# Performance work log

Measured on AMD Instinct MI355X. Metric: run time of the kernel, lower is better.

## Reference

```python
import jax, jax.numpy as jnp
import numpy as np

B, S, H = 64, 512, 256
H2 = 2 * H
TOPK, TRUNC = 5, 100
EPS = 1e-7
TMAX = S + 1  # h_old slot 0 is the initial zero state; one slot appended per step
NEG = -1e9


def setup_inputs() -> dict:
    key = jax.random.key(0)
    ks = jax.random.split(key, 8)
    p = lambda k, shape: jax.random.normal(k, shape, jnp.float32) * 0.08
    return {
        "x": jax.random.normal(ks[0], (B, S), jnp.float32),
        "W_ih_f": p(ks[1], (4 * H, 1)),
        "W_hh_f": p(ks[2], (4 * H, H)),
        "b_f": p(ks[3], (4 * H,)),
        "W_ih_b": p(ks[4], (4 * H, 1)),
        "W_hh_b": p(ks[5], (4 * H, H)),
        "b_b": p(ks[6], (4 * H,)),
        "w_t": p(ks[7], (4 * H, 1)),
    }


def _lstm_cell(xt, h, c, W_ih, W_hh, b):
    # torch.nn.LSTMCell: gates ordered i, f, g, o
    g = xt @ W_ih.T + h @ W_hh.T + b
    i, f, gg, o = jnp.split(g, 4, axis=1)
    i, f, o = jax.nn.sigmoid(i), jax.nn.sigmoid(f), jax.nn.sigmoid(o)
    c2 = f * c + i * jnp.tanh(gg)
    return o * jnp.tanh(c2), c2


def _forward(x, W_ih_f, W_hh_f, b_f, W_ih_b, W_hh_b, b_b, w_t):
    # tanh(cat(h_comb, h_old)) @ w_t == tanh(h_comb)@w1 + tanh(h_old)@w2
    w1, w2 = w_t[:H2, 0], w_t[H2:, 0]
    pos = jnp.arange(TMAX)

    h0 = jnp.zeros((B, H), jnp.float32)
    h_old0 = jnp.zeros((B, TMAX, H2), jnp.float32)   # slot 0 = initial zeros (valid)
    th_old0 = jnp.zeros((B, TMAX, H2), jnp.float32)  # cached tanh(h_old)
    carry0 = (h0, h0, h0, h0, h_old0, th_old0,
              jnp.zeros((B, H2), jnp.float32), jnp.zeros((B, TMAX), jnp.float32))

    def step(carry, i):
        h_f, c_f, h_b, c_b, h_old, th_old, _, _ = carry
        trunc = ((i + 1) % TRUNC) == 0  # TBPTT detach point
        sg = lambda a: jnp.where(trunc, jax.lax.stop_gradient(a), a)
        h_f, c_f, h_b, c_b = sg(h_f), sg(c_f), sg(h_b), sg(c_b)

        xf = jax.lax.dynamic_slice_in_dim(x, i, 1, axis=1)          # [B,1]
        xb = jax.lax.dynamic_slice_in_dim(x, S - 1 - i, 1, axis=1)  # [B,1]
        h_f, c_f = _lstm_cell(xf, h_f, c_f, W_ih_f, W_hh_f, b_f)
        h_b, c_b = _lstm_cell(xb, h_b, c_b, W_ih_b, W_hh_b, b_b)
        h_comb = jnp.concatenate([h_f, h_b], axis=1)  # [B,2H]

        rs = i + 1                    # remember_size before append
        valid = pos < rs              # [TMAX]
        s = jnp.tanh(h_comb) @ w1[:, None] + th_old @ w2  # [B,1]+[B,TMAX]
        s_m = jnp.where(valid[None, :], s, NEG)

        # Sparse_attention: subtract k-th largest, clamp at 0, renormalize
        delta = jax.lax.top_k(s_m, TOPK)[0][:, -1] + EPS  # [B]
        w_sp = jnp.clip(s_m - delta[:, None], 0.0, None)
        w_sp = w_sp / (w_sp.sum(axis=1, keepdims=True) + EPS)
        w_raw = jnp.where(valid[None, :], s, 0.0)  # time_step <= top_k branch
        attn_w = jnp.where(rs <= TOPK, w_raw, w_sp)  # [B,TMAX]

        attn_c = jnp.einsum('bt,bth->bh', attn_w, h_old)  # weighted sum of cache
        h_new = h_comb + attn_c

        h_old = jax.lax.dynamic_update_slice_in_dim(
            h_old, h_new[:, None, :], i + 1, axis=1)
        th_old = jax.lax.dynamic_update_slice_in_dim(
            th_old, jnp.tanh(h_new)[:, None, :], i + 1, axis=1)
        return (h_f, c_f, h_b, c_b, h_old, th_old, attn_c, attn_w), None

    carry, _ = jax.lax.scan(step, carry0, jnp.arange(S))
    attn_c, attn_w = carry[6], carry[7]
    # last step: remember_size == S, torch returns [B, S, 1]
    return attn_c, attn_w[:, :S, None]


def reference(x, W_ih_f, W_hh_f, b_f, W_ih_b, W_hh_b, b_b, w_t):
    return _forward(x, W_ih_f, W_hh_f, b_f, W_ih_b, W_hh_b, b_b, w_t)
```

## Files before the change

### kernel.cpp

```cpp
#include <hip/hip_runtime.h>
#include <math.h>

#define BB    64
#define SS    512
#define HH    256
#define HH2   512
#define TMAXX 513
#define NTOP  5
#define EPSF  1e-7f

#if defined(__has_builtin)
#if __has_builtin(__builtin_amdgcn_sdot4)
#define HAVE_SDOT4 1
#endif
#endif

__device__ __forceinline__ int dot4i8_(unsigned a, int b, int c) {
#ifdef HAVE_SDOT4
  return __builtin_amdgcn_sdot4((int)a, b, c, false);
#else
  int acc = c;
#pragma unroll
  for (int j = 0; j < 4; ++j) {
    int av = (int)(signed char)(a >> (8 * j));
    int bv = (int)(signed char)(((unsigned)b) >> (8 * j));
    acc += av * bv;
  }
  return acc;
#endif
}


__global__ void init_kernel(const float* __restrict__ Whh_f, const float* __restrict__ Whh_b,
                            uint4* __restrict__ wq, float* __restrict__ scales) {
  int t = blockIdx.x * blockDim.x + threadIdx.x;
  if (t >= 2048) return;
  int d = t >> 10, row = t & 1023;
  const float* src = (d ? Whh_b : Whh_f) + (size_t)row * HH;
  float m = 1e-20f;
  for (int k = 0; k < HH; ++k) m = fmaxf(m, fabsf(src[k]));
  float inv = 127.f / m;
  scales[t] = m * (1.f / 16129.f);
  for (int kq4 = 0; kq4 < 16; ++kq4) {
    unsigned u[4];
#pragma unroll
    for (int w = 0; w < 4; ++w) {
      unsigned uu = 0;
#pragma unroll
      for (int j = 0; j < 4; ++j) {
        float q = rintf(src[kq4 * 16 + w * 4 + j] * inv);
        q = fminf(fmaxf(q, -127.f), 127.f);
        uu |= ((unsigned)(((int)q) & 0xff)) << (8 * j);
      }
      u[w] = uu;
    }
    wq[(size_t)(d * 16 + kq4) * 1024 + row] = make_uint4(u[0], u[1], u[2], u[3]);
  }
}

__global__ __launch_bounds__(1024, 4)
void lstm_kernel(const float* __restrict__ x,
                 const float* __restrict__ wihf, const float* __restrict__ bf,
                 const float* __restrict__ wihb, const float* __restrict__ bb_,
                 const uint4* __restrict__ wq, const float* __restrict__ scales,
                 float* __restrict__ hcomb) {
  const int r   = blockIdx.x >> 1;
  const int d   = blockIdx.x & 1;
  const int tid = threadIdx.x;

  __shared__ float x_lds[SS];
  __shared__ float gates_lds[1024];
  __shared__ int   h_ints[64];

  for (int t = tid; t < SS; t += 1024) x_lds[t] = x[(size_t)r * SS + t];
  if (tid < 64) h_ints[tid] = 0;

  const float wihv = d ? wihb[tid] : wihf[tid];
  const float bv   = d ? bb_[tid]  : bf[tid];
  const float sc   = scales[d * 1024 + tid];
  float c = 0.f;
  float* hout = hcomb + (size_t)r * SS * HH2 + d * HH;

  uint4 w[16];
  {
    const uint4* wbase = wq + (size_t)(d * 16) * 1024 + tid;
#pragma unroll
    for (int q = 0; q < 16; ++q) w[q] = wbase[(size_t)q * 1024];
  }
  __syncthreads();

  for (int i = 0; i < SS; ++i) {
    int a0 = 0, a1 = 0, a2 = 0, a3 = 0;
    const int4* hp = (const int4*)h_ints;
#pragma unroll
    for (int q = 0; q < 16; ++q) {
      int4 h4 = hp[q];
      a0 = dot4i8_(w[q].x, h4.x, a0);
      a1 = dot4i8_(w[q].y, h4.y, a1);
      a2 = dot4i8_(w[q].z, h4.z, a2);
      a3 = dot4i8_(w[q].w, h4.w, a3);
    }
    float xv = x_lds[d ? (SS - 1 - i) : i];
    gates_lds[tid] = (float)(a0 + a1 + a2 + a3) * sc + fmaf(xv, wihv, bv);
    __syncthreads();
    if (tid < HH) {
      float gi = gates_lds[tid];
      float gf = gates_lds[HH + tid];
      float gg = gates_lds[2 * HH + tid];
      float go = gates_lds[3 * HH + tid];
      float ig = 1.f / (1.f + expf(-gi));
      float fg = 1.f / (1.f + expf(-gf));
      float og = 1.f / (1.f + expf(-go));
      c = fg * c + ig * tanhf(gg);
      float hn = og * tanhf(c);
      hout[(size_t)i * HH2 + tid] = hn;
      ((signed char*)h_ints)[tid] = (signed char)(int)rintf(hn * 127.f);
    }
    __syncthreads();
  }
}

__global__ __launch_bounds__(512, 1)
void attn_kernel(const float* __restrict__ w_t, float* __restrict__ hcomb,
                 float* __restrict__ out) {
  const int b = blockIdx.x;
  const int e = threadIdx.x;
  const int lane = e & 63, wv = e >> 6;
  float* hrow = hcomb + (size_t)b * SS * HH2;

  __shared__ float w1_l[HH2], w2_l[HH2];
  __shared__ float tw_l[TMAXX];
  __shared__ float t5v[NTOP];
  __shared__ int   t5i[NTOP];
  __shared__ float redp[8];
  __shared__ float sh_s1, sh_tw5, sh_inv;
  __shared__ float sh_wk[4];
  __shared__ int   sh_ik[4];

  w1_l[e] = w_t[e];
  w2_l[e] = w_t[HH2 + e];
  if (e == 0) { tw_l[0] = 0.f; t5v[0] = 0.f; t5i[0] = 0; }
  int t5cnt = 1;
  __syncthreads();

  for (int i = 0; i < SS; ++i) {
    float hc = hrow[(size_t)i * HH2 + e];
    if (i < NTOP) {
      float v = tanhf(hc) * w1_l[e];
#pragma unroll
      for (int m = 32; m >= 1; m >>= 1) v += __shfl_xor(v, m, 64);
      if (lane == 0) redp[wv] = v;
      __syncthreads();
      if (e == 0) {
        float s = 0.f;
#pragma unroll
        for (int q = 0; q < 8; ++q) s += redp[q];
        sh_s1 = s;
      }
    }
    if (i >= NTOP && e == 0) {
      float tw5 = t5v[4];
      float rk[4], rsum = 0.f;
#pragma unroll
      for (int k = 0; k < 4; ++k) {
        float rr = t5v[k] - tw5 - EPSF;
        rk[k] = rr > 0.f ? rr : 0.f;
        rsum += rk[k];
      }
      float inv = 1.f / (rsum + EPSF);
#pragma unroll
      for (int k = 0; k < 4; ++k) { sh_wk[k] = rk[k] * inv; sh_ik[k] = t5i[k]; }
      sh_tw5 = tw5; sh_inv = inv;
    }
    __syncthreads();
    float acc = 0.f;
    if (i >= NTOP) {
#pragma unroll
      for (int k = 0; k < 4; ++k) {
        float w = sh_wk[k];
        int   t = sh_ik[k];
        if (w > 0.f && t > 0)
          acc = fmaf(w, hrow[(size_t)(t - 1) * HH2 + e], acc);
      }
    } else {
      float s1 = sh_s1;
      for (int t = 1; t <= i; ++t)
        acc = fmaf(s1 + tw_l[t], hrow[(size_t)(t - 1) * HH2 + e], acc);
    }
    float hn = hc + acc;
    hrow[(size_t)i * HH2 + e] = hn;
    float v2 = tanhf(hn) * w2_l[e];
#pragma unroll
    for (int m = 32; m >= 1; m >>= 1) v2 += __shfl_xor(v2, m, 64);
    if (lane == 0) redp[wv] = v2;
    if (i == SS - 1) {
      out[(size_t)b * HH2 + e] = acc;
      float rr = tw_l[e] - sh_tw5 - EPSF;
      out[(size_t)BB * HH2 + (size_t)b * SS + e] = rr > 0.f ? rr * sh_inv : 0.f;
    }
    __syncthreads();
    if (e == 0) {
      float v = 0.f;
#pragma unroll
      for (int q = 0; q < 8; ++q) v += redp[q];
      int idx = i + 1;
      tw_l[idx] = v;
      if (t5cnt < NTOP) {
        int p = t5cnt++;
        t5v[p] = v; t5i[p] = idx;
        while (p > 0 && t5v[p] > t5v[p - 1]) {
          float tv = t5v[p]; t5v[p] = t5v[p - 1]; t5v[p - 1] = tv;
          int   ti = t5i[p]; t5i[p] = t5i[p - 1]; t5i[p - 1] = ti;
          --p;
        }
      } else if (v > t5v[4]) {
        t5v[4] = v; t5i[4] = idx;
        int p = 4;
        while (p > 0 && t5v[p] > t5v[p - 1]) {
          float tv = t5v[p]; t5v[p] = t5v[p - 1]; t5v[p - 1] = tv;
          int   ti = t5i[p]; t5i[p] = t5i[p - 1]; t5i[p - 1] = ti;
          --p;
        }
      }
    }
    __syncthreads();
  }
}

extern "C" void kernel_launch(void* const* d_in, const int* in_sizes, int n_in,
                              void* d_out, int out_size, void* d_ws, size_t ws_size,
                              hipStream_t stream) {
  const float* x     = (const float*)d_in[0];
  const float* Wih_f = (const float*)d_in[1];
  const float* Whh_f = (const float*)d_in[2];
  const float* b_f   = (const float*)d_in[3];
  const float* Wih_b = (const float*)d_in[4];
  const float* Whh_b = (const float*)d_in[5];
  const float* b_b   = (const float*)d_in[6];
  const float* w_t   = (const float*)d_in[7];
  float* out = (float*)d_out;

  char* ws = (char*)d_ws;
  uint4*  wq     = (uint4*)ws;
  float*  scales = (float*)(ws + (1 << 20));
  float*  hcomb  = (float*)(ws + (4 << 20));

  init_kernel<<<8, 256, 0, stream>>>(Whh_f, Whh_b, wq, scales);
  lstm_kernel<<<2 * BB, 1024, 0, stream>>>(x, Wih_f, b_f, Wih_b, b_b,
                                           wq, scales, hcomb);
  attn_kernel<<<BB, 512, 0, stream>>>(w_t, hcomb, out);
}
```

Before: 1.346 ms.

## Restructure LSTM to one thread per hidden unit and attention to single-wave registers

After: 1.445 ms. +7.3%, slower.

```diff
diff --git a/kernel.cpp b/kernel.cpp
--- a/kernel.cpp
+++ b/kernel.cpp
@@ -58,172 +58,187 @@
   }
 }
 
-__global__ __launch_bounds__(1024, 4)
+__global__ __launch_bounds__(256, 1)
 void lstm_kernel(const float* __restrict__ x,
                  const float* __restrict__ wihf, const float* __restrict__ bf,
                  const float* __restrict__ wihb, const float* __restrict__ bb_,
                  const uint4* __restrict__ wq, const float* __restrict__ scales,
                  float* __restrict__ hcomb) {
-  const int r   = blockIdx.x >> 1;
-  const int d   = blockIdx.x & 1;
-  const int tid = threadIdx.x;
+  const int r = blockIdx.x >> 1;
+  const int d = blockIdx.x & 1;
+  const int e = threadIdx.x;
 
   __shared__ float x_lds[SS];
-  __shared__ float gates_lds[1024];
-  __shared__ int   h_ints[64];
-
-  for (int t = tid; t < SS; t += 1024) x_lds[t] = x[(size_t)r * SS + t];
-  if (tid < 64) h_ints[tid] = 0;
-
-  const float wihv = d ? wihb[tid] : wihf[tid];
-  const float bv   = d ? bb_[tid]  : bf[tid];
-  const float sc   = scales[d * 1024 + tid];
+  __shared__ int   hbuf[2][64];
+
+  for (int t = e; t < SS; t += 256) x_lds[t] = x[(size_t)r * SS + t];
+  if (e < 64) hbuf[0][e] = 0;
+
+  float wih[4], bias[4], sc[4];
+#pragma unroll
+  for (int g = 0; g < 4; ++g) {
+    int row = g * HH + e;
+    wih[g]  = d ? wihb[row] : wihf[row];
+    bias[g] = d ? bb_[row]  : bf[row];
+    sc[g]   = scales[d * 1024 + row];
+  }
+  uint4 w[4][16];
+#pragma unroll
+  for (int g = 0; g < 4; ++g) {
+    const uint4* wb = wq + (size_t)(d * 16) * 1024 + g * HH + e;
+#pragma unroll
+    for (int q = 0; q < 16; ++q) w[g][q] = wb[(size_t)q * 1024];
+  }
   float c = 0.f;
   float* hout = hcomb + (size_t)r * SS * HH2 + d * HH;
-
-  uint4 w[16];
-  {
-    const uint4* wbase = wq + (size_t)(d * 16) * 1024 + tid;
-#pragma unroll
-    for (int q = 0; q < 16; ++q) w[q] = wbase[(size_t)q * 1024];
-  }
   __syncthreads();
 
+  int cur = 0;
   for (int i = 0; i < SS; ++i) {
+    const int4* hp = (const int4*)hbuf[cur];
     int a0 = 0, a1 = 0, a2 = 0, a3 = 0;
-    const int4* hp = (const int4*)h_ints;
 #pragma unroll
     for (int q = 0; q < 16; ++q) {
       int4 h4 = hp[q];
-      a0 = dot4i8_(w[q].x, h4.x, a0);
-      a1 = dot4i8_(w[q].y, h4.y, a1);
-      a2 = dot4i8_(w[q].z, h4.z, a2);
-      a3 = dot4i8_(w[q].w, h4.w, a3);
+      a0 = dot4i8_(w[0][q].x, h4.x, a0); a0 = dot4i8_(w[0][q].y, h4.y, a0);
+      a0 = dot4i8_(w[0][q].z, h4.z, a0); a0 = dot4i8_(w[0][q].w, h4.w, a0);
+      a1 = dot4i8_(w[1][q].x, h4.x, a1); a1 = dot4i8_(w[1][q].y, h4.y, a1);
+      a1 = dot4i8_(w[1][q].z, h4.z, a1); a1 = dot4i8_(w[1][q].w, h4.w, a1);
+      a2 = dot4i8_(w[2][q].x, h4.x, a2); a2 = dot4i8_(w[2][q].y, h4.y, a2);
+      a2 = dot4i8_(w[2][q].z, h4.z, a2); a2 = dot4i8_(w[2][q].w, h4.w, a2);
+      a3 = dot4i8_(w[3][q].x, h4.x, a3); a3 = dot4i8_(w[3][q].y, h4.y, a3);
+      a3 = dot4i8_(w[3][q].z, h4.z, a3); a3 = dot4i8_(w[3][q].w, h4.w, a3);
     }
     float xv = x_lds[d ? (SS - 1 - i) : i];
-    gates_lds[tid] = (float)(a0 + a1 + a2 + a3) * sc + fmaf(xv, wihv, bv);
+    float gi = (float)a0 * sc[0] + fmaf(xv, wih[0], bias[0]);
+    float gf = (float)a1 * sc[1] + fmaf(xv, wih[1], bias[1]);
+    float gg = (float)a2 * sc[2] + fmaf(xv, wih[2], bias[2]);
+    float go = (float)a3 * sc[3] + fmaf(xv, wih[3], bias[3]);
+    float ig = 1.f / (1.f + expf(-gi));
+    float fg = 1.f / (1.f + expf(-gf));
+    float og = 1.f / (1.f + expf(-go));
+    c = fg * c + ig * tanhf(gg);
+    float hn = og * tanhf(c);
+    hout[(size_t)i * HH2 + e] = hn;
+    ((signed char*)hbuf[cur ^ 1])[e] = (signed char)(int)rintf(hn * 127.f);
+    cur ^= 1;
     __syncthreads();
-    if (tid < HH) {
-      float gi = gates_lds[tid];
-      float gf = gates_lds[HH + tid];
-      float gg = gates_lds[2 * HH + tid];
-      float go = gates_lds[3 * HH + tid];
-      float ig = 1.f / (1.f + expf(-gi));
-      float fg = 1.f / (1.f + expf(-gf));
-      float og = 1.f / (1.f + expf(-go));
-      c = fg * c + ig * tanhf(gg);
-      float hn = og * tanhf(c);
-      hout[(size_t)i * HH2 + tid] = hn;
-      ((signed char*)h_ints)[tid] = (signed char)(int)rintf(hn * 127.f);
-    }
-    __syncthreads();
-  }
-}
-
-__global__ __launch_bounds__(512, 1)
-void attn_kernel(const float* __restrict__ w_t, float* __restrict__ hcomb,
+  }
+}
+
+__global__ __launch_bounds__(64, 1)
+void attn_kernel(const float* __restrict__ w_t, const float* __restrict__ hcomb,
                  float* __restrict__ out) {
   const int b = blockIdx.x;
-  const int e = threadIdx.x;
-  const int lane = e & 63, wv = e >> 6;
-  float* hrow = hcomb + (size_t)b * SS * HH2;
-
-  __shared__ float w1_l[HH2], w2_l[HH2];
+  const int l = threadIdx.x;
+  const float* hrow = hcomb + (size_t)b * SS * HH2;
+
   __shared__ float tw_l[TMAXX];
-  __shared__ float t5v[NTOP];
-  __shared__ int   t5i[NTOP];
-  __shared__ float redp[8];
-  __shared__ float sh_s1, sh_tw5, sh_inv;
-  __shared__ float sh_wk[4];
-  __shared__ int   sh_ik[4];
-
-  w1_l[e] = w_t[e];
-  w2_l[e] = w_t[HH2 + e];
-  if (e == 0) { tw_l[0] = 0.f; t5v[0] = 0.f; t5i[0] = 0; }
-  int t5cnt = 1;
-  __syncthreads();
+
+  const float4 w1a = *(const float4*)(w_t + 4 * l);
+  const float4 w1b = *(const float4*)(w_t + HH + 4 * l);
+  const float4 w2a = *(const float4*)(w_t + HH2 + 4 * l);
+  const float4 w2b = *(const float4*)(w_t + HH2 + HH + 4 * l);
+
+  float t5v[5] = {0.f, -1e30f, -1e30f, -1e30f, -1e30f};
+  int   t5s[5] = {0, 1, 2, 3, 4};
+  int   t5cnt  = 1;
+  float4 z4 = make_float4(0.f, 0.f, 0.f, 0.f);
+  float4 sA0 = z4, sA1 = z4, sA2 = z4, sA3 = z4, sA4 = z4;
+  float4 sB0 = z4, sB1 = z4, sB2 = z4, sB3 = z4, sB4 = z4;
+  if (l == 0) tw_l[0] = 0.f;
+
+  float4 ha = *(const float4*)(hrow + 4 * l);
+  float4 hb = *(const float4*)(hrow + HH + 4 * l);
+  float tw5 = 0.f, inv = 0.f;
+  float4 aA = z4, aB = z4;
 
   for (int i = 0; i < SS; ++i) {
-    float hc = hrow[(size_t)i * HH2 + e];
-    if (i < NTOP) {
-      float v = tanhf(hc) * w1_l[e];
-#pragma unroll
-      for (int m = 32; m >= 1; m >>= 1) v += __shfl_xor(v, m, 64);
-      if (lane == 0) redp[wv] = v;
-      __syncthreads();
-      if (e == 0) {
-        float s = 0.f;
-#pragma unroll
-        for (int q = 0; q < 8; ++q) s += redp[q];
-        sh_s1 = s;
+    float4 na = z4, nb = z4;
+    if (i + 1 < SS) {
+      na = *(const float4*)(hrow + (size_t)(i + 1) * HH2 + 4 * l);
+      nb = *(const float4*)(hrow + (size_t)(i + 1) * HH2 + HH + 4 * l);
+    }
+    float wr[5];
+    if (i >= NTOP) {
+      tw5 = t5v[4];
+      float rk0 = fmaxf(t5v[0] - tw5 - EPSF, 0.f);
+      float rk1 = fmaxf(t5v[1] - tw5 - EPSF, 0.f);
+      float rk2 = fmaxf(t5v[2] - tw5 - EPSF, 0.f);
+      float rk3 = fmaxf(t5v[3] - tw5 - EPSF, 0.f);
+      inv = 1.f / (rk0 + rk1 + rk2 + rk3 + EPSF);
+      wr[0] = rk0 * inv; wr[1] = rk1 * inv; wr[2] = rk2 * inv; wr[3] = rk3 * inv;
+      wr[4] = 0.f;
+    } else {
+      float s = tanhf(ha.x) * w1a.x + tanhf(ha.y) * w1a.y +
+                tanhf(ha.z) * w1a.z + tanhf(ha.w) * w1a.w +
+                tanhf(hb.x) * w1b.x + tanhf(hb.y) * w1b.y +
+                tanhf(hb.z) * w1b.z + tanhf(hb.w) * w1b.w;
+#pragma unroll
+      for (int m = 1; m < 64; m <<= 1) s += __shfl_xor(s, m, 64);
+#pragma unroll
+      for (int k = 0; k < 5; ++k) wr[k] = (k < t5cnt) ? (s + t5v[k]) : 0.f;
+    }
+    float ws0 = 0.f, ws1 = 0.f, ws2 = 0.f, ws3 = 0.f, ws4 = 0.f;
+#pragma unroll
+    for (int k = 0; k < 5; ++k) {
+      float wv = wr[k]; int s2 = t5s[k];
+      ws0 += (s2 == 0) ? wv : 0.f;
+      ws1 += (s2 == 1) ? wv : 0.f;
+      ws2 += (s2 == 2) ? wv : 0.f;
+      ws3 += (s2 == 3) ? wv : 0.f;
+      ws4 += (s2 == 4) ? wv : 0.f;
+    }
+    aA.x = ws0*sA0.x + ws1*sA1.x + ws2*sA2.x + ws3*sA3.x + ws4*sA4.x;
+    aA.y = ws0*sA0.y + ws1*sA1.y + ws2*sA2.y + ws3*sA3.y + ws4*sA4.y;
+    aA.z = ws0*sA0.z + ws1*sA1.z + ws2*sA2.z + ws3*sA3.z + ws4*sA4.z;
+    aA.w = ws0*sA0.w + ws1*sA1.w + ws2*sA2.w + ws3*sA3.w + ws4*sA4.w;
+    aB.x = ws0*sB0.x + ws1*sB1.x + ws2*sB2.x + ws3*sB3.x + ws4*sB4.x;
+    aB.y = ws0*sB0.y + ws1*sB1.y + ws2*sB2.y + ws3*sB3.y + ws4*sB4.y;
+    aB.z = ws0*sB0.z + ws1*sB1.z + ws2*sB2.z + ws3*sB3.z + ws4*sB4.z;
+    aB.w = ws0*sB0.w + ws1*sB1.w + ws2*sB2.w + ws3*sB3.w + ws4*sB4.w;
+    float4 hnA, hnB;
+    hnA.x = ha.x + aA.x; hnA.y = ha.y + aA.y; hnA.z = ha.z + aA.z; hnA.w = ha.w + aA.w;
+    hnB.x = hb.x + aB.x; hnB.y = hb.y + aB.y; hnB.z = hb.z + aB.z; hnB.w = hb.w + aB.w;
+    float v = tanhf(hnA.x) * w2a.x + tanhf(hnA.y) * w2a.y +
+              tanhf(hnA.z) * w2a.z + tanhf(hnA.w) * w2a.w +
+              tanhf(hnB.x) * w2b.x + tanhf(hnB.y) * w2b.y +
+              tanhf(hnB.z) * w2b.z + tanhf(hnB.w) * w2b.w;
+#pragma unroll
+    for (int m = 1; m < 64; m <<= 1) v += __shfl_xor(v, m, 64);
+    if (l == 0) tw_l[i + 1] = v;
+    bool full = (t5cnt >= 5);
+    bool ins  = !full || (v > t5v[4]);
+    if (ins) {
+      int p    = full ? 4 : t5cnt;
+      int slot = full ? t5s[4] : t5cnt;
+#pragma unroll
+      for (int k = 0; k < 5; ++k) if (k == p) { t5v[k] = v; t5s[k] = slot; }
+      if (slot == 0)      { sA0 = hnA; sB0 = hnB; }
+      else if (slot == 1) { sA1 = hnA; sB1 = hnB; }
+      else if (slot == 2) { sA2 = hnA; sB2 = hnB; }
+      else if (slot == 3) { sA3 = hnA; sB3 = hnB; }
+      else                { sA4 = hnA; sB4 = hnB; }
+      if (!full) ++t5cnt;
+#pragma unroll
+      for (int k = 4; k >= 1; --k) {
+        bool sw = (k <= p) && (t5v[k] > t5v[k - 1]);
+        float v0 = t5v[k - 1], v1 = t5v[k];
+        int   s0 = t5s[k - 1], s1 = t5s[k];
+        t5v[k] = sw ? v0 : v1;  t5v[k - 1] = sw ? v1 : v0;
+        t5s[k] = sw ? s0 : s1;  t5s[k - 1] = sw ? s1 : s0;
       }
     }
-    if (i >= NTOP && e == 0) {
-      float tw5 = t5v[4];
-      float rk[4], rsum = 0.f;
-#pragma unroll
-      for (int k = 0; k < 4; ++k) {
-        float rr = t5v[k] - tw5 - EPSF;
-        rk[k] = rr > 0.f ? rr : 0.f;
-        rsum += rk[k];
-      }
-      float inv = 1.f / (rsum + EPSF);
-#pragma unroll
-      for (int k = 0; k < 4; ++k) { sh_wk[k] = rk[k] * inv; sh_ik[k] = t5i[k]; }
-      sh_tw5 = tw5; sh_inv = inv;
-    }
-    __syncthreads();
-    float acc = 0.f;
-    if (i >= NTOP) {
-#pragma unroll
-      for (int k = 0; k < 4; ++k) {
-        float w = sh_wk[k];
-        int   t = sh_ik[k];
-        if (w > 0.f && t > 0)
-          acc = fmaf(w, hrow[(size_t)(t - 1) * HH2 + e], acc);
-      }
-    } else {
-      float s1 = sh_s1;
-      for (int t = 1; t <= i; ++t)
-        acc = fmaf(s1 + tw_l[t], hrow[(size_t)(t - 1) * HH2 + e], acc);
-    }
-    float hn = hc + acc;
-    hrow[(size_t)i * HH2 + e] = hn;
-    float v2 = tanhf(hn) * w2_l[e];
-#pragma unroll
-    for (int m = 32; m >= 1; m >>= 1) v2 += __shfl_xor(v2, m, 64);
-    if (lane == 0) redp[wv] = v2;
-    if (i == SS - 1) {
-      out[(size_t)b * HH2 + e] = acc;
-      float rr = tw_l[e] - sh_tw5 - EPSF;
-      out[(size_t)BB * HH2 + (size_t)b * SS + e] = rr > 0.f ? rr * sh_inv : 0.f;
-    }
-    __syncthreads();
-    if (e == 0) {
-      float v = 0.f;
-#pragma unroll
-      for (int q = 0; q < 8; ++q) v += redp[q];
-      int idx = i + 1;
-      tw_l[idx] = v;
-      if (t5cnt < NTOP) {
-        int p = t5cnt++;
-        t5v[p] = v; t5i[p] = idx;
-        while (p > 0 && t5v[p] > t5v[p - 1]) {
-          float tv = t5v[p]; t5v[p] = t5v[p - 1]; t5v[p - 1] = tv;
-          int   ti = t5i[p]; t5i[p] = t5i[p - 1]; t5i[p - 1] = ti;
-          --p;
-        }
-      } else if (v > t5v[4]) {
-        t5v[4] = v; t5i[4] = idx;
-        int p = 4;
-        while (p > 0 && t5v[p] > t5v[p - 1]) {
-          float tv = t5v[p]; t5v[p] = t5v[p - 1]; t5v[p - 1] = tv;
-          int   ti = t5i[p]; t5i[p] = t5i[p - 1]; t5i[p - 1] = ti;
-          --p;
-        }
-      }
-    }
-    __syncthreads();
+    ha = na; hb = nb;
+  }
+  *(float4*)(out + (size_t)b * HH2 + 4 * l)      = aA;
+  *(float4*)(out + (size_t)b * HH2 + HH + 4 * l) = aB;
+  float* ow = out + (size_t)BB * HH2 + (size_t)b * SS;
+#pragma unroll
+  for (int j = 0; j < 8; ++j) {
+    int t = j * 64 + l;
+    float rr = tw_l[t] - tw5 - EPSF;
+    ow[t] = rr > 0.f ? rr * inv : 0.f;
   }
 }
 
@@ -246,7 +261,7 @@
   float*  hcomb  = (float*)(ws + (4 << 20));
 
   init_kernel<<<8, 256, 0, stream>>>(Whh_f, Whh_b, wq, scales);
-  lstm_kernel<<<2 * BB, 1024, 0, stream>>>(x, Wih_f, b_f, Wih_b, b_b,
-                                           wq, scales, hcomb);
-  attn_kernel<<<BB, 512, 0, stream>>>(w_t, hcomb, out);
-}
+  lstm_kernel<<<2 * BB, 256, 0, stream>>>(x, Wih_f, b_f, Wih_b, b_b,
+                                          wq, scales, hcomb);
+  attn_kernel<<<BB, 64, 0, stream>>>(w_t, hcomb, out);
+}
```
